# Kernel tuning notes

Hardware: AMD Instinct MI355X
Metric: run time of the kernel (lower is better)

The kernel has to match this reference:

```python
import jax, jax.numpy as jnp
import numpy as np

N_NODES = 10000
N_EDGES = 320000
D = 256
VOCAB = 28
NEG_SLOPE = 0.2


def _gat_conv(x, ei_src, ei_dst, W, a_src, a_dst, b):
    """PyG GATConv with heads=1, concat=True, self-loops already in ei."""
    h = x @ W                                  # [N, D]
    alpha_s = h @ a_src                        # [N]
    alpha_d = h @ a_dst                        # [N]
    logits = jax.nn.leaky_relu(alpha_s[ei_src] + alpha_d[ei_dst], NEG_SLOPE)  # [E]
    # numerically stable edge softmax per destination node
    m = jax.ops.segment_max(logits, ei_dst, num_segments=N_NODES)
    e = jnp.exp(logits - m[ei_dst])
    denom = jax.ops.segment_sum(e, ei_dst, num_segments=N_NODES)
    alpha = e / denom[ei_dst]                  # [E]
    msgs = alpha[:, None] * h[ei_src]          # [E, D]
    out = jax.ops.segment_sum(msgs, ei_dst, num_segments=N_NODES)
    return out + b


def setup_inputs() -> dict:
    key = jax.random.key(0)
    ks = jax.random.split(key, 16)
    x = jax.random.randint(ks[0], (N_NODES, 1), 0, VOCAB, dtype=jnp.int64)
    edge_index = jax.random.randint(ks[1], (2, N_EDGES), 0, N_NODES, dtype=jnp.int64)
    edge_attr = jax.random.uniform(ks[2], (N_EDGES,), dtype=jnp.float32)
    sc = 1.0 / np.sqrt(D)
    inp = {"x": x, "edge_index": edge_index, "edge_attr": edge_attr,
           "emb": jax.random.normal(ks[3], (VOCAB, D), jnp.float32)}
    for i, k0 in enumerate([4, 7, 10]):
        l = i + 1
        inp[f"W{l}"] = jax.random.normal(ks[k0], (D, D), jnp.float32) * sc
        inp[f"a_src{l}"] = jax.random.normal(ks[k0 + 1], (D,), jnp.float32) * sc
        inp[f"a_dst{l}"] = jax.random.normal(ks[k0 + 2], (D,), jnp.float32) * sc
        inp[f"b{l}"] = jnp.zeros((D,), jnp.float32)
    return inp


def reference(x, edge_index, edge_attr, emb,
              W1, a_src1, a_dst1, b1,
              W2, a_src2, a_dst2, b2,
              W3, a_src3, a_dst3, b3):
    # edge_attr is ignored by GATConv (edge_dim=None), matching PyG behavior.
    # add self loops (PyG default add_self_loops=True)
    loops = jnp.arange(N_NODES, dtype=edge_index.dtype)
    ei_src = jnp.concatenate([edge_index[0], loops])
    ei_dst = jnp.concatenate([edge_index[1], loops])

    h = emb[x.squeeze(-1)]                     # [N, D]
    h = jax.nn.relu(_gat_conv(h, ei_src, ei_dst, W1, a_src1, a_dst1, b1)) + h
    h = jax.nn.relu(_gat_conv(h, ei_src, ei_dst, W2, a_src2, a_dst2, b2)) + h
    out = jax.nn.relu(_gat_conv(h, ei_src, ei_dst, W3, a_src3, a_dst3, b3)) + h
    return out
```

## Files before the change

### kernel.cpp

```cpp
#include <hip/hip_runtime.h>
#include <hip/hip_bf16.h>

#define N_NODES 10000
#define N_EDGES 320000
#define E_TOT (N_EDGES + N_NODES)
#define D 256
#define VOCAB 28
#define NEG 0.2f
#define CAP 96

typedef __attribute__((ext_vector_type(8))) short bf16x8;
typedef __attribute__((ext_vector_type(4))) float f32x4;

__device__ inline float blo(unsigned u) { return __uint_as_float(u << 16); }
__device__ inline float bhi(unsigned u) { return __uint_as_float(u & 0xFFFF0000u); }
__device__ inline unsigned short f2bu(float x) {
  __hip_bfloat16 b = __float2bfloat16(x);
  return *reinterpret_cast<unsigned short*>(&b);
}

__global__ __launch_bounds__(256) void scatter_kernel(const int* __restrict__ ei,
                                                      int* __restrict__ counts,
                                                      int* __restrict__ csr) {
  int e = blockIdx.x * 256 + threadIdx.x;
  if (e >= E_TOT) return;
  int src, dst;
  if (e < N_EDGES) { src = ei[e]; dst = ei[N_EDGES + e]; }
  else             { src = e - N_EDGES; dst = src; }
  int pos = atomicAdd(&counts[dst], 1);
  csr[dst * CAP + pos] = src;
}

__global__ __launch_bounds__(256) void convw_kernel(const float* __restrict__ W0,
                                                    const float* __restrict__ W1,
                                                    const float* __restrict__ W2,
                                                    const float* __restrict__ emb,
                                                    unsigned short* __restrict__ T0,
                                                    unsigned short* __restrict__ T1,
                                                    unsigned short* __restrict__ T2,
                                                    unsigned short* __restrict__ emb_b,
                                                    float4* __restrict__ zbase) {
  __shared__ float t[64][65];
  int tid = threadIdx.x;
  if (blockIdx.x >= 49) {
    zbase[(blockIdx.x - 49) * 256 + tid] = float4{0.f, 0.f, 0.f, 0.f};
    return;
  }
  if (blockIdx.x == 48) {
    for (int i = tid; i < VOCAB * D; i += 256) emb_b[i] = f2bu(emb[i]);
    return;
  }
  int l = blockIdx.x >> 4;
  const float* W = (l == 0) ? W0 : (l == 1) ? W1 : W2;
  unsigned short* Wt = (l == 0) ? T0 : (l == 1) ? T1 : T2;
  int sub = blockIdx.x & 15;
  int bk = (sub & 3) * 64;
  int bn = (sub >> 2) * 64;
  int row = tid >> 2;
  int cq = (tid & 3) * 16;
#pragma unroll
  for (int i = 0; i < 4; ++i) {
    float4 v = *reinterpret_cast<const float4*>(W + (size_t)(bk + row) * D + bn + cq + i * 4);
    t[row][cq + i * 4 + 0] = v.x; t[row][cq + i * 4 + 1] = v.y;
    t[row][cq + i * 4 + 2] = v.z; t[row][cq + i * 4 + 3] = v.w;
  }
  __syncthreads();
#pragma unroll
  for (int i = 0; i < 16; ++i)
    Wt[(size_t)(bn + row) * D + bk + cq + i] = f2bu(t[cq + i][row]);
}

__global__ __launch_bounds__(256) void gemm_kernel(const unsigned short* __restrict__ Asrc,
                                                   const int* __restrict__ xv,
                                                   const unsigned short* __restrict__ emb_b,
                                                   const unsigned short* __restrict__ Bt,
                                                   unsigned short* __restrict__ C,
                                                   const float* __restrict__ a_src,
                                                   const float* __restrict__ a_dst,
                                                   float* __restrict__ al_s,
                                                   float* __restrict__ al_d) {
  __shared__ unsigned short As[64][264];
  __shared__ unsigned short Bs[64][264];
  __shared__ int xs[64];
  int t = threadIdx.x;
  int bm = blockIdx.x * 64;
  int bn = blockIdx.y * 64;
  int lane = t & 63, wid = t >> 6;
  int wr = (wid >> 1) * 32, wc = (wid & 1) * 32;
  int fr = lane & 15, fk = (lane >> 4) * 8;

  if (xv && t < 64) {
    int gr = bm + t;
    xs[t] = (gr < N_NODES) ? xv[gr] : 0;
  }
  if (xv) __syncthreads();

#pragma unroll
  for (int c = t; c < 2048; c += 256) {
    int row = c >> 5, cc = (c & 31) * 8;
    int gr = bm + row;
    uint4 v = {0u, 0u, 0u, 0u};
    if (gr < N_NODES) {
      const unsigned short* src = xv ? (emb_b + (size_t)xs[row] * D)
                                     : (Asrc + (size_t)gr * D);
      v = *reinterpret_cast<const uint4*>(src + cc);
    }
    *reinterpret_cast<uint4*>(&As[row][cc]) = v;
    uint4 w = *reinterpret_cast<const uint4*>(Bt + (size_t)(bn + row) * D + cc);
    *reinterpret_cast<uint4*>(&Bs[row][cc]) = w;
  }
  __syncthreads();

  f32x4 acc[2][2] = {};
#pragma unroll
  for (int ks = 0; ks < 8; ++ks) {
    bf16x8 a0 = *reinterpret_cast<const bf16x8*>(&As[wr + fr][ks * 32 + fk]);
    bf16x8 a1 = *reinterpret_cast<const bf16x8*>(&As[wr + 16 + fr][ks * 32 + fk]);
    bf16x8 b0 = *reinterpret_cast<const bf16x8*>(&Bs[wc + fr][ks * 32 + fk]);
    bf16x8 b1 = *reinterpret_cast<const bf16x8*>(&Bs[wc + 16 + fr][ks * 32 + fk]);
    acc[0][0] = __builtin_amdgcn_mfma_f32_16x16x32_bf16(a0, b0, acc[0][0], 0, 0, 0);
    acc[0][1] = __builtin_amdgcn_mfma_f32_16x16x32_bf16(a0, b1, acc[0][1], 0, 0, 0);
    acc[1][0] = __builtin_amdgcn_mfma_f32_16x16x32_bf16(a1, b0, acc[1][0], 0, 0, 0);
    acc[1][1] = __builtin_amdgcn_mfma_f32_16x16x32_bf16(a1, b1, acc[1][1], 0, 0, 0);
  }

  int orow = (lane >> 4) * 4;
#pragma unroll
  for (int m = 0; m < 2; ++m)
#pragma unroll
    for (int n = 0; n < 2; ++n)
#pragma unroll
      for (int r = 0; r < 4; ++r) {
        int gr = bm + wr + m * 16 + orow + r;
        if (gr < N_NODES)
          C[(size_t)gr * D + bn + wc + n * 16 + fr] = f2bu(acc[m][n][r]);
      }
  float as0 = a_src[bn + wc + fr];
  float as1 = a_src[bn + wc + 16 + fr];
  float ad0 = a_dst[bn + wc + fr];
  float ad1 = a_dst[bn + wc + 16 + fr];
#pragma unroll
  for (int m = 0; m < 2; ++m)
#pragma unroll
    for (int r = 0; r < 4; ++r) {
      float vs = acc[m][0][r] * as0 + acc[m][1][r] * as1;
      float vd = acc[m][0][r] * ad0 + acc[m][1][r] * ad1;
#pragma unroll
      for (int off = 8; off; off >>= 1) {
        vs += __shfl_xor(vs, off);
        vd += __shfl_xor(vd, off);
      }
      if ((lane & 15) == 0) {
        int gr = bm + wr + m * 16 + orow + r;
        if (gr < N_NODES) {
          atomicAdd(&al_s[gr], vs);
          atomicAdd(&al_d[gr], vd);
        }
      }
    }
}

__global__ __launch_bounds__(256) void agg_kernel(const int* __restrict__ csr,
                                                  const int* __restrict__ counts,
                                                  const float* __restrict__ al_s,
                                                  const float* __restrict__ al_d,
                                                  const unsigned short* __restrict__ hlin,
                                                  const float* __restrict__ bias,
                                                  const float* __restrict__ h_prev,
                                                  const int* __restrict__ xv,
                                                  const float* __restrict__ emb,
                                                  float* __restrict__ out_f,
                                                  unsigned short* __restrict__ out_b) {
  __shared__ int   ssh[4][CAP];
  __shared__ float wsh[4][CAP];
  int wid = threadIdx.x >> 6, lane = threadIdx.x & 63;
  int dst = blockIdx.x * 4 + wid;
  if (dst >= N_NODES) return;
  int cnt = counts[dst];
  const int* rowp = csr + (size_t)dst * CAP;
  float ad = al_d[dst];

  float m = -1e30f;
  for (int j = lane; j < cnt; j += 64) {
    int s = rowp[j];
    ssh[wid][j] = s;
    float v = al_s[s] + ad;
    v = (v >= 0.f) ? v : NEG * v;
    wsh[wid][j] = v;
    m = fmaxf(m, v);
  }
#pragma unroll
  for (int off = 32; off; off >>= 1) m = fmaxf(m, __shfl_xor(m, off));

  float denom = 0.f;
  for (int j = lane; j < cnt; j += 64) {
    float w = __expf(wsh[wid][j] - m);
    wsh[wid][j] = w;
    denom += w;
  }
#pragma unroll
  for (int off = 32; off; off >>= 1) denom += __shfl_xor(denom, off);
  float inv = 1.0f / denom;

  int half = lane >> 5, fl = lane & 31;
  const unsigned short* hb_base = hlin + fl * 8;
  float a0 = 0.f, a1 = 0.f, a2 = 0.f, a3 = 0.f;
  float a4 = 0.f, a5 = 0.f, a6 = 0.f, a7 = 0.f;
  int j = 0;
  for (; j + 8 <= cnt; j += 8) {
    int s0 = ssh[wid][j + 0 + half];
    int s1 = ssh[wid][j + 2 + half];
    int s2 = ssh[wid][j + 4 + half];
    int s3 = ssh[wid][j + 6 + half];
    float w0 = wsh[wid][j + 0 + half];
    float w1 = wsh[wid][j + 2 + half];
    float w2 = wsh[wid][j + 4 + half];
    float w3 = wsh[wid][j + 6 + half];
    uint4 q0 = *reinterpret_cast<const uint4*>(hb_base + (size_t)s0 * D);
    uint4 q1 = *reinterpret_cast<const uint4*>(hb_base + (size_t)s1 * D);
    uint4 q2 = *reinterpret_cast<const uint4*>(hb_base + (size_t)s2 * D);
    uint4 q3 = *reinterpret_cast<const uint4*>(hb_base + (size_t)s3 * D);
    a0 += w0 * blo(q0.x); a1 += w0 * bhi(q0.x); a2 += w0 * blo(q0.y); a3 += w0 * bhi(q0.y);
    a4 += w0 * blo(q0.z); a5 += w0 * bhi(q0.z); a6 += w0 * blo(q0.w); a7 += w0 * bhi(q0.w);
    a0 += w1 * blo(q1.x); a1 += w1 * bhi(q1.x); a2 += w1 * blo(q1.y); a3 += w1 * bhi(q1.y);
    a4 += w1 * blo(q1.z); a5 += w1 * bhi(q1.z); a6 += w1 * blo(q1.w); a7 += w1 * bhi(q1.w);
    a0 += w2 * blo(q2.x); a1 += w2 * bhi(q2.x); a2 += w2 * blo(q2.y); a3 += w2 * bhi(q2.y);
    a4 += w2 * blo(q2.z); a5 += w2 * bhi(q2.z); a6 += w2 * blo(q2.w); a7 += w2 * bhi(q2.w);
    a0 += w3 * blo(q3.x); a1 += w3 * bhi(q3.x); a2 += w3 * blo(q3.y); a3 += w3 * bhi(q3.y);
    a4 += w3 * blo(q3.z); a5 += w3 * bhi(q3.z); a6 += w3 * blo(q3.w); a7 += w3 * bhi(q3.w);
  }
  for (; j < cnt; j += 2) {
    int jj = j + half;
    bool valid = jj < cnt;
    int s0 = ssh[wid][valid ? jj : 0];
    float w0 = valid ? wsh[wid][jj] : 0.f;
    uint4 q0 = *reinterpret_cast<const uint4*>(hb_base + (size_t)s0 * D);
    a0 += w0 * blo(q0.x); a1 += w0 * bhi(q0.x); a2 += w0 * blo(q0.y); a3 += w0 * bhi(q0.y);
    a4 += w0 * blo(q0.z); a5 += w0 * bhi(q0.z); a6 += w0 * blo(q0.w); a7 += w0 * bhi(q0.w);
  }
  a0 += __shfl_xor(a0, 32); a1 += __shfl_xor(a1, 32);
  a2 += __shfl_xor(a2, 32); a3 += __shfl_xor(a3, 32);
  a4 += __shfl_xor(a4, 32); a5 += __shfl_xor(a5, 32);
  a6 += __shfl_xor(a6, 32); a7 += __shfl_xor(a7, 32);
  float b0 = half ? a4 : a0, b1 = half ? a5 : a1;
  float b2 = half ? a6 : a2, b3 = half ? a7 : a3;
  int fb = fl * 8 + half * 4;
  const float* hp_row = h_prev ? (h_prev + (size_t)dst * D)
                               : (emb + (size_t)xv[dst] * D);
  float4 bb = *reinterpret_cast<const float4*>(bias + fb);
  float4 hp = *reinterpret_cast<const float4*>(hp_row + fb);
  float o0 = fmaxf(b0 * inv + bb.x, 0.f) + hp.x;
  float o1 = fmaxf(b1 * inv + bb.y, 0.f) + hp.y;
  float o2 = fmaxf(b2 * inv + bb.z, 0.f) + hp.z;
  float o3 = fmaxf(b3 * inv + bb.w, 0.f) + hp.w;
  float4 o = {o0, o1, o2, o3};
  *reinterpret_cast<float4*>(out_f + (size_t)dst * D + fb) = o;
  if (out_b) {
    uint2 p;
    p.x = (unsigned)f2bu(o0) | ((unsigned)f2bu(o1) << 16);
    p.y = (unsigned)f2bu(o2) | ((unsigned)f2bu(o3) << 16);
    *reinterpret_cast<uint2*>(out_b + (size_t)dst * D + fb) = p;
  }
}

extern "C" void kernel_launch(void* const* d_in, const int* in_sizes, int n_in,
                              void* d_out, int out_size, void* d_ws, size_t ws_size,
                              hipStream_t stream) {
  const int*   x   = (const int*)d_in[0];
  const int*   ei  = (const int*)d_in[1];
  const float* emb = (const float*)d_in[3];
  const float* W[3]    = {(const float*)d_in[4],  (const float*)d_in[8],  (const float*)d_in[12]};
  const float* asrc[3] = {(const float*)d_in[5],  (const float*)d_in[9],  (const float*)d_in[13]};
  const float* adst[3] = {(const float*)d_in[6],  (const float*)d_in[10], (const float*)d_in[14]};
  const float* bias[3] = {(const float*)d_in[7],  (const float*)d_in[11], (const float*)d_in[15]};

  char* ws = (char*)d_ws;
  float*          h    = (float*)(ws);
  unsigned short* hb   = (unsigned short*)(ws + 10240000);
  unsigned short* hlin = (unsigned short*)(ws + 15360000);
  unsigned short* Wt[3] = {(unsigned short*)(ws + 20480000),
                           (unsigned short*)(ws + 20611072),
                           (unsigned short*)(ws + 20742144)};
  float* al_s[3] = {(float*)(ws + 20873216), (float*)(ws + 20914176), (float*)(ws + 20955136)};
  float* al_d[3] = {(float*)(ws + 20996096), (float*)(ws + 21037056), (float*)(ws + 21078016)};
  int* counts = (int*)(ws + 21118976);
  int* csr    = (int*)(ws + 21241856);
  unsigned short* emb_b = (unsigned short*)(ws + 25081856);

  convw_kernel<<<119, 256, 0, stream>>>(W[0], W[1], W[2], emb,
                                        Wt[0], Wt[1], Wt[2], emb_b,
                                        (float4*)(ws + 20873216));

  scatter_kernel<<<(E_TOT + 255) / 256, 256, 0, stream>>>(ei, counts, csr);

  dim3 gemm_grid((N_NODES + 63) / 64, D / 64);
  for (int l = 0; l < 3; ++l) {
    const unsigned short* Ain = (l == 0) ? (const unsigned short*)nullptr : hb;
    const int* xg = (l == 0) ? x : (const int*)nullptr;
    gemm_kernel<<<gemm_grid, 256, 0, stream>>>(Ain, xg, emb_b, Wt[l], hlin,
                                               asrc[l], adst[l], al_s[l], al_d[l]);
    float* outp = (l == 2) ? (float*)d_out : h;
    unsigned short* outb = (l == 2) ? (unsigned short*)nullptr : hb;
    const float* hp = (l == 0) ? (const float*)nullptr : h;
    agg_kernel<<<(N_NODES + 3) / 4, 256, 0, stream>>>(csr, counts, al_s[l], al_d[l],
                                                      hlin, bias[l], hp, x, emb,
                                                      outp, outb);
  }
}
```

Measured before the change: 137.6 us.

## Fuse all stages into one cooperative persistent kernel with grid syncs

Replaces the eight separate launches (weight conversion, CSR scatter, three GEMM plus aggregation pairs) with a single cooperative persistent kernel that separates phases with grid.sync. The first GEMM runs alongside the edge scatter on disjoint block subsets. The GEMM tile now loops over K in 64-wide chunks with a smaller shared buffer, which lowers LDS use and raises occupancy but adds syncthreads per K step. The aim is to remove launch gaps and tail effects, in exchange for the cost of grid-wide barriers and a fixed grid size.

```diff
diff --git a/kernel.cpp b/kernel.cpp
--- a/kernel.cpp
+++ b/kernel.cpp
@@ -1,5 +1,8 @@
 #include <hip/hip_runtime.h>
 #include <hip/hip_bf16.h>
+#include <hip/hip_cooperative_groups.h>
+
+namespace cg = cooperative_groups;
 
 #define N_NODES 10000
 #define N_EDGES 320000
@@ -8,6 +11,10 @@
 #define VOCAB 28
 #define NEG 0.2f
 #define CAP 96
+#define NTILE_M 157
+#define NTILES (NTILE_M * 4)
+#define NGROUP 2500
+#define SMEM_BYTES 18688
 
 typedef __attribute__((ext_vector_type(8))) short bf16x8;
 typedef __attribute__((ext_vector_type(4))) float f32x4;
@@ -19,109 +26,73 @@
   return *reinterpret_cast<unsigned short*>(&b);
 }
 
-__global__ __launch_bounds__(256) void scatter_kernel(const int* __restrict__ ei,
-                                                      int* __restrict__ counts,
-                                                      int* __restrict__ csr) {
-  int e = blockIdx.x * 256 + threadIdx.x;
-  if (e >= E_TOT) return;
-  int src, dst;
-  if (e < N_EDGES) { src = ei[e]; dst = ei[N_EDGES + e]; }
-  else             { src = e - N_EDGES; dst = src; }
-  int pos = atomicAdd(&counts[dst], 1);
-  csr[dst * CAP + pos] = src;
-}
-
-__global__ __launch_bounds__(256) void convw_kernel(const float* __restrict__ W0,
-                                                    const float* __restrict__ W1,
-                                                    const float* __restrict__ W2,
-                                                    const float* __restrict__ emb,
-                                                    unsigned short* __restrict__ T0,
-                                                    unsigned short* __restrict__ T1,
-                                                    unsigned short* __restrict__ T2,
-                                                    unsigned short* __restrict__ emb_b,
-                                                    float4* __restrict__ zbase) {
-  __shared__ float t[64][65];
-  int tid = threadIdx.x;
-  if (blockIdx.x >= 49) {
-    zbase[(blockIdx.x - 49) * 256 + tid] = float4{0.f, 0.f, 0.f, 0.f};
-    return;
-  }
-  if (blockIdx.x == 48) {
-    for (int i = tid; i < VOCAB * D; i += 256) emb_b[i] = f2bu(emb[i]);
-    return;
-  }
-  int l = blockIdx.x >> 4;
-  const float* W = (l == 0) ? W0 : (l == 1) ? W1 : W2;
-  unsigned short* Wt = (l == 0) ? T0 : (l == 1) ? T1 : T2;
-  int sub = blockIdx.x & 15;
-  int bk = (sub & 3) * 64;
-  int bn = (sub >> 2) * 64;
-  int row = tid >> 2;
-  int cq = (tid & 3) * 16;
-#pragma unroll
-  for (int i = 0; i < 4; ++i) {
-    float4 v = *reinterpret_cast<const float4*>(W + (size_t)(bk + row) * D + bn + cq + i * 4);
-    t[row][cq + i * 4 + 0] = v.x; t[row][cq + i * 4 + 1] = v.y;
-    t[row][cq + i * 4 + 2] = v.z; t[row][cq + i * 4 + 3] = v.w;
-  }
-  __syncthreads();
-#pragma unroll
-  for (int i = 0; i < 16; ++i)
-    Wt[(size_t)(bn + row) * D + bk + cq + i] = f2bu(t[cq + i][row]);
-}
-
-__global__ __launch_bounds__(256) void gemm_kernel(const unsigned short* __restrict__ Asrc,
-                                                   const int* __restrict__ xv,
-                                                   const unsigned short* __restrict__ emb_b,
-                                                   const unsigned short* __restrict__ Bt,
-                                                   unsigned short* __restrict__ C,
-                                                   const float* __restrict__ a_src,
-                                                   const float* __restrict__ a_dst,
-                                                   float* __restrict__ al_s,
-                                                   float* __restrict__ al_d) {
-  __shared__ unsigned short As[64][264];
-  __shared__ unsigned short Bs[64][264];
-  __shared__ int xs[64];
+struct MegaArgs {
+  const int* x; const int* ei;
+  const float *emb, *W0, *W1, *W2;
+  const float *as0, *ad0, *b0, *as1, *ad1, *b1, *as2, *ad2, *b2;
+  unsigned short *T0, *T1, *T2, *emb_b, *hb, *hlin;
+  float *h;
+  float *als0, *ald0, *als1, *ald1, *als2, *ald2;
+  int *counts, *csr;
+  float4* zbase;
+  float* dout;
+};
+
+__device__ void gemm_tile(int tile, const unsigned short* __restrict__ Asrc,
+                          const int* __restrict__ xv,
+                          const unsigned short* __restrict__ emb_b,
+                          const unsigned short* __restrict__ Bt,
+                          unsigned short* __restrict__ C,
+                          const float* __restrict__ a_src, const float* __restrict__ a_dst,
+                          float* __restrict__ al_s, float* __restrict__ al_d,
+                          char* smem) {
+  unsigned short (*As)[72] = (unsigned short(*)[72])smem;
+  unsigned short (*Bs)[72] = (unsigned short(*)[72])(smem + 9216);
+  int* xs = (int*)(smem + 18432);
   int t = threadIdx.x;
-  int bm = blockIdx.x * 64;
-  int bn = blockIdx.y * 64;
+  int bm = (tile % NTILE_M) * 64;
+  int bn = (tile / NTILE_M) * 64;
   int lane = t & 63, wid = t >> 6;
   int wr = (wid >> 1) * 32, wc = (wid & 1) * 32;
   int fr = lane & 15, fk = (lane >> 4) * 8;
 
-  if (xv && t < 64) {
-    int gr = bm + t;
-    xs[t] = (gr < N_NODES) ? xv[gr] : 0;
-  }
-  if (xv) __syncthreads();
-
-#pragma unroll
-  for (int c = t; c < 2048; c += 256) {
-    int row = c >> 5, cc = (c & 31) * 8;
-    int gr = bm + row;
-    uint4 v = {0u, 0u, 0u, 0u};
-    if (gr < N_NODES) {
-      const unsigned short* src = xv ? (emb_b + (size_t)xs[row] * D)
-                                     : (Asrc + (size_t)gr * D);
-      v = *reinterpret_cast<const uint4*>(src + cc);
-    }
-    *reinterpret_cast<uint4*>(&As[row][cc]) = v;
-    uint4 w = *reinterpret_cast<const uint4*>(Bt + (size_t)(bn + row) * D + cc);
-    *reinterpret_cast<uint4*>(&Bs[row][cc]) = w;
-  }
-  __syncthreads();
+  if (xv) {
+    if (t < 64) {
+      int gr = bm + t;
+      xs[t] = (gr < N_NODES) ? xv[gr] : 0;
+    }
+    __syncthreads();
+  }
 
   f32x4 acc[2][2] = {};
-#pragma unroll
-  for (int ks = 0; ks < 8; ++ks) {
-    bf16x8 a0 = *reinterpret_cast<const bf16x8*>(&As[wr + fr][ks * 32 + fk]);
-    bf16x8 a1 = *reinterpret_cast<const bf16x8*>(&As[wr + 16 + fr][ks * 32 + fk]);
-    bf16x8 b0 = *reinterpret_cast<const bf16x8*>(&Bs[wc + fr][ks * 32 + fk]);
-    bf16x8 b1 = *reinterpret_cast<const bf16x8*>(&Bs[wc + 16 + fr][ks * 32 + fk]);
-    acc[0][0] = __builtin_amdgcn_mfma_f32_16x16x32_bf16(a0, b0, acc[0][0], 0, 0, 0);
-    acc[0][1] = __builtin_amdgcn_mfma_f32_16x16x32_bf16(a0, b1, acc[0][1], 0, 0, 0);
-    acc[1][0] = __builtin_amdgcn_mfma_f32_16x16x32_bf16(a1, b0, acc[1][0], 0, 0, 0);
-    acc[1][1] = __builtin_amdgcn_mfma_f32_16x16x32_bf16(a1, b1, acc[1][1], 0, 0, 0);
+  for (int k0 = 0; k0 < D; k0 += 64) {
+#pragma unroll
+    for (int c = t; c < 512; c += 256) {
+      int row = c >> 3, cc = (c & 7) * 8;
+      int gr = bm + row;
+      uint4 v = {0u, 0u, 0u, 0u};
+      if (gr < N_NODES) {
+        const unsigned short* src = xv ? (emb_b + (size_t)xs[row] * D)
+                                       : (Asrc + (size_t)gr * D);
+        v = *reinterpret_cast<const uint4*>(src + k0 + cc);
+      }
+      *reinterpret_cast<uint4*>(&As[row][cc]) = v;
+      uint4 w = *reinterpret_cast<const uint4*>(Bt + (size_t)(bn + row) * D + k0 + cc);
+      *reinterpret_cast<uint4*>(&Bs[row][cc]) = w;
+    }
+    __syncthreads();
+#pragma unroll
+    for (int ks = 0; ks < 2; ++ks) {
+      bf16x8 a0 = *reinterpret_cast<const bf16x8*>(&As[wr + fr][ks * 32 + fk]);
+      bf16x8 a1 = *reinterpret_cast<const bf16x8*>(&As[wr + 16 + fr][ks * 32 + fk]);
+      bf16x8 b0 = *reinterpret_cast<const bf16x8*>(&Bs[wc + fr][ks * 32 + fk]);
+      bf16x8 b1 = *reinterpret_cast<const bf16x8*>(&Bs[wc + 16 + fr][ks * 32 + fk]);
+      acc[0][0] = __builtin_amdgcn_mfma_f32_16x16x32_bf16(a0, b0, acc[0][0], 0, 0, 0);
+      acc[0][1] = __builtin_amdgcn_mfma_f32_16x16x32_bf16(a0, b1, acc[0][1], 0, 0, 0);
+      acc[1][0] = __builtin_amdgcn_mfma_f32_16x16x32_bf16(a1, b0, acc[1][0], 0, 0, 0);
+      acc[1][1] = __builtin_amdgcn_mfma_f32_16x16x32_bf16(a1, b1, acc[1][1], 0, 0, 0);
+    }
+    __syncthreads();
   }
 
   int orow = (lane >> 4) * 4;
@@ -160,22 +131,17 @@
     }
 }
 
-__global__ __launch_bounds__(256) void agg_kernel(const int* __restrict__ csr,
-                                                  const int* __restrict__ counts,
-                                                  const float* __restrict__ al_s,
-                                                  const float* __restrict__ al_d,
-                                                  const unsigned short* __restrict__ hlin,
-                                                  const float* __restrict__ bias,
-                                                  const float* __restrict__ h_prev,
-                                                  const int* __restrict__ xv,
-                                                  const float* __restrict__ emb,
-                                                  float* __restrict__ out_f,
-                                                  unsigned short* __restrict__ out_b) {
-  __shared__ int   ssh[4][CAP];
-  __shared__ float wsh[4][CAP];
+__device__ void agg_group(int g, const int* __restrict__ csr, const int* __restrict__ counts,
+                          const float* __restrict__ al_s, const float* __restrict__ al_d,
+                          const unsigned short* __restrict__ hlin,
+                          const float* __restrict__ bias, const float* __restrict__ h_prev,
+                          const int* __restrict__ xv, const float* __restrict__ emb,
+                          float* __restrict__ out_f, unsigned short* __restrict__ out_b,
+                          char* smem) {
+  int (*ssh)[CAP] = (int(*)[CAP])smem;
+  float (*wsh)[CAP] = (float(*)[CAP])(smem + 4 * CAP * 4);
   int wid = threadIdx.x >> 6, lane = threadIdx.x & 63;
-  int dst = blockIdx.x * 4 + wid;
-  if (dst >= N_NODES) return;
+  int dst = g * 4 + wid;
   int cnt = counts[dst];
   const int* rowp = csr + (size_t)dst * CAP;
   float ad = al_d[dst];
@@ -263,47 +229,126 @@
   }
 }
 
+__global__ __launch_bounds__(256) void mega_kernel(MegaArgs a) {
+  __shared__ __align__(16) char smem[SMEM_BYTES];
+  cg::grid_group grid = cg::this_grid();
+  const int bid = blockIdx.x;
+  const int G = gridDim.x;
+  const int tid = threadIdx.x;
+
+  if (bid < 48) {
+    float (*t)[65] = (float(*)[65])smem;
+    int l = bid >> 4;
+    const float* W = (l == 0) ? a.W0 : (l == 1) ? a.W1 : a.W2;
+    unsigned short* Wt = (l == 0) ? a.T0 : (l == 1) ? a.T1 : a.T2;
+    int sub = bid & 15;
+    int bk = (sub & 3) * 64;
+    int bn = (sub >> 2) * 64;
+    int row = tid >> 2;
+    int cq = (tid & 3) * 16;
+#pragma unroll
+    for (int i = 0; i < 4; ++i) {
+      float4 v = *reinterpret_cast<const float4*>(W + (size_t)(bk + row) * D + bn + cq + i * 4);
+      t[row][cq + i * 4 + 0] = v.x; t[row][cq + i * 4 + 1] = v.y;
+      t[row][cq + i * 4 + 2] = v.z; t[row][cq + i * 4 + 3] = v.w;
+    }
+    __syncthreads();
+#pragma unroll
+    for (int i = 0; i < 16; ++i)
+      Wt[(size_t)(bn + row) * D + bk + cq + i] = f2bu(t[cq + i][row]);
+  } else if (bid == 48) {
+    for (int i = tid; i < VOCAB * D; i += 256) a.emb_b[i] = f2bu(a.emb[i]);
+  } else {
+    for (int i = (bid - 49) * 256 + tid; i < 17920; i += (G - 49) * 256)
+      a.zbase[i] = float4{0.f, 0.f, 0.f, 0.f};
+  }
+  grid.sync();
+
+  {
+    int Gg = (3 * G) / 4;
+    if (Gg > NTILES) Gg = NTILES;
+    if (bid < Gg) {
+      for (int tile = bid; tile < NTILES; tile += Gg)
+        gemm_tile(tile, nullptr, a.x, a.emb_b, a.T0, a.hlin,
+                  a.as0, a.ad0, a.als0, a.ald0, smem);
+    } else {
+      int nb = G - Gg;
+      for (int e = (bid - Gg) * 256 + tid; e < E_TOT; e += nb * 256) {
+        int src, dst;
+        if (e < N_EDGES) { src = a.ei[e]; dst = a.ei[N_EDGES + e]; }
+        else             { src = e - N_EDGES; dst = src; }
+        int pos = atomicAdd(&a.counts[dst], 1);
+        a.csr[dst * CAP + pos] = src;
+      }
+    }
+  }
+  grid.sync();
+
+  for (int g = bid; g < NGROUP; g += G)
+    agg_group(g, a.csr, a.counts, a.als0, a.ald0, a.hlin, a.b0,
+              nullptr, a.x, a.emb, a.h, a.hb, smem);
+  grid.sync();
+
+  for (int tile = bid; tile < NTILES; tile += G)
+    gemm_tile(tile, a.hb, nullptr, a.emb_b, a.T1, a.hlin,
+              a.as1, a.ad1, a.als1, a.ald1, smem);
+  grid.sync();
+
+  for (int g = bid; g < NGROUP; g += G)
+    agg_group(g, a.csr, a.counts, a.als1, a.ald1, a.hlin, a.b1,
+              a.h, a.x, a.emb, a.h, a.hb, smem);
+  grid.sync();
+
+  for (int tile = bid; tile < NTILES; tile += G)
+    gemm_tile(tile, a.hb, nullptr, a.emb_b, a.T2, a.hlin,
+              a.as2, a.ad2, a.als2, a.ald2, smem);
+  grid.sync();
+
+  for (int g = bid; g < NGROUP; g += G)
+    agg_group(g, a.csr, a.counts, a.als2, a.ald2, a.hlin, a.b2,
+              a.h, a.x, a.emb, a.dout, nullptr, smem);
+}
+
 extern "C" void kernel_launch(void* const* d_in, const int* in_sizes, int n_in,
                               void* d_out, int out_size, void* d_ws, size_t ws_size,
                               hipStream_t stream) {
-  const int*   x   = (const int*)d_in[0];
-  const int*   ei  = (const int*)d_in[1];
-  const float* emb = (const float*)d_in[3];
-  const float* W[3]    = {(const float*)d_in[4],  (const float*)d_in[8],  (const float*)d_in[12]};
-  const float* asrc[3] = {(const float*)d_in[5],  (const float*)d_in[9],  (const float*)d_in[13]};
-  const float* adst[3] = {(const float*)d_in[6],  (const float*)d_in[10], (const float*)d_in[14]};
-  const float* bias[3] = {(const float*)d_in[7],  (const float*)d_in[11], (const float*)d_in[15]};
-
   char* ws = (char*)d_ws;
-  float*          h    = (float*)(ws);
-  unsigned short* hb   = (unsigned short*)(ws + 10240000);
-  unsigned short* hlin = (unsigned short*)(ws + 15360000);
-  unsigned short* Wt[3] = {(unsigned short*)(ws + 20480000),
-                           (unsigned short*)(ws + 20611072),
-                           (unsigned short*)(ws + 20742144)};
-  float* al_s[3] = {(float*)(ws + 20873216), (float*)(ws + 20914176), (float*)(ws + 20955136)};
-  float* al_d[3] = {(float*)(ws + 20996096), (float*)(ws + 21037056), (float*)(ws + 21078016)};
-  int* counts = (int*)(ws + 21118976);
-  int* csr    = (int*)(ws + 21241856);
-  unsigned short* emb_b = (unsigned short*)(ws + 25081856);
-
-  convw_kernel<<<119, 256, 0, stream>>>(W[0], W[1], W[2], emb,
-                                        Wt[0], Wt[1], Wt[2], emb_b,
-                                        (float4*)(ws + 20873216));
-
-  scatter_kernel<<<(E_TOT + 255) / 256, 256, 0, stream>>>(ei, counts, csr);
-
-  dim3 gemm_grid((N_NODES + 63) / 64, D / 64);
-  for (int l = 0; l < 3; ++l) {
-    const unsigned short* Ain = (l == 0) ? (const unsigned short*)nullptr : hb;
-    const int* xg = (l == 0) ? x : (const int*)nullptr;
-    gemm_kernel<<<gemm_grid, 256, 0, stream>>>(Ain, xg, emb_b, Wt[l], hlin,
-                                               asrc[l], adst[l], al_s[l], al_d[l]);
-    float* outp = (l == 2) ? (float*)d_out : h;
-    unsigned short* outb = (l == 2) ? (unsigned short*)nullptr : hb;
-    const float* hp = (l == 0) ? (const float*)nullptr : h;
-    agg_kernel<<<(N_NODES + 3) / 4, 256, 0, stream>>>(csr, counts, al_s[l], al_d[l],
-                                                      hlin, bias[l], hp, x, emb,
-                                                      outp, outb);
-  }
-}
+  MegaArgs a;
+  a.x   = (const int*)d_in[0];
+  a.ei  = (const int*)d_in[1];
+  a.emb = (const float*)d_in[3];
+  a.W0 = (const float*)d_in[4];  a.as0 = (const float*)d_in[5];
+  a.ad0 = (const float*)d_in[6]; a.b0 = (const float*)d_in[7];
+  a.W1 = (const float*)d_in[8];  a.as1 = (const float*)d_in[9];
+  a.ad1 = (const float*)d_in[10]; a.b1 = (const float*)d_in[11];
+  a.W2 = (const float*)d_in[12]; a.as2 = (const float*)d_in[13];
+  a.ad2 = (const float*)d_in[14]; a.b2 = (const float*)d_in[15];
+
+  a.h     = (float*)(ws);
+  a.hb    = (unsigned short*)(ws + 10240000);
+  a.hlin  = (unsigned short*)(ws + 15360000);
+  a.T0    = (unsigned short*)(ws + 20480000);
+  a.T1    = (unsigned short*)(ws + 20611072);
+  a.T2    = (unsigned short*)(ws + 20742144);
+  a.als0  = (float*)(ws + 20873216);
+  a.als1  = (float*)(ws + 20914176);
+  a.als2  = (float*)(ws + 20955136);
+  a.ald0  = (float*)(ws + 20996096);
+  a.ald1  = (float*)(ws + 21037056);
+  a.ald2  = (float*)(ws + 21078016);
+  a.counts = (int*)(ws + 21118976);
+  a.zbase  = (float4*)(ws + 20873216);
+  a.csr    = (int*)(ws + 21241856);
+  a.emb_b  = (unsigned short*)(ws + 25081856);
+  a.dout   = (float*)d_out;
+
+  int bpc = 0;
+  hipError_t err = hipOccupancyMaxActiveBlocksPerMultiprocessor(&bpc, mega_kernel, 256, 0);
+  if (err != hipSuccess || bpc < 1) bpc = 2;
+  int G = bpc * 256;
+  if (G > 2048) G = 2048;
+  if (G < 256) G = 256;
+
+  void* kargs[] = { &a };
+  hipLaunchCooperativeKernel(mega_kernel, dim3(G), dim3(256), kargs, 0, stream);
+}
```

Measured after the change: 491.4 us. 257% more time.

## Loop GEMM over all output column tiles per block, drop attention-score atomics

Applied to the files above, without the earlier changes.

Each GEMM block now loads its 64-row A tile once and loops over the four 64-column B tiles, instead of launching a 2D grid that reloads A for each column tile. The per-row attention dot products are accumulated in registers, reduced through shared memory, and written directly, which removes the atomicAdds and the need to zero al_s/al_d. As a result the convw kernel launches fewer blocks and only zeroes counts. The trade-off is a grid 4x smaller (157 blocks), which may underfill the GPU, plus serialized B loads with extra barriers inside each block.

```diff
diff --git a/kernel.cpp b/kernel.cpp
--- a/kernel.cpp
+++ b/kernel.cpp
@@ -8,6 +8,7 @@
 #define VOCAB 28
 #define NEG 0.2f
 #define CAP 96
+#define NBLK 157
 
 typedef __attribute__((ext_vector_type(8))) short bf16x8;
 typedef __attribute__((ext_vector_type(4))) float f32x4;
@@ -81,19 +82,23 @@
                                                    float* __restrict__ al_d) {
   __shared__ unsigned short As[64][264];
   __shared__ unsigned short Bs[64][264];
+  __shared__ float red_s[8][32];
+  __shared__ float red_d[8][32];
   __shared__ int xs[64];
   int t = threadIdx.x;
   int bm = blockIdx.x * 64;
-  int bn = blockIdx.y * 64;
   int lane = t & 63, wid = t >> 6;
-  int wr = (wid >> 1) * 32, wc = (wid & 1) * 32;
+  int wrb = (wid >> 1) * 32, wcb = (wid & 1) * 32;
   int fr = lane & 15, fk = (lane >> 4) * 8;
-
-  if (xv && t < 64) {
-    int gr = bm + t;
-    xs[t] = (gr < N_NODES) ? xv[gr] : 0;
-  }
-  if (xv) __syncthreads();
+  int orow = (lane >> 4) * 4;
+
+  if (xv) {
+    if (t < 64) {
+      int gr = bm + t;
+      xs[t] = (gr < N_NODES) ? xv[gr] : 0;
+    }
+    __syncthreads();
+  }
 
 #pragma unroll
   for (int c = t; c < 2048; c += 256) {
@@ -106,58 +111,79 @@
       v = *reinterpret_cast<const uint4*>(src + cc);
     }
     *reinterpret_cast<uint4*>(&As[row][cc]) = v;
-    uint4 w = *reinterpret_cast<const uint4*>(Bt + (size_t)(bn + row) * D + cc);
-    *reinterpret_cast<uint4*>(&Bs[row][cc]) = w;
-  }
-  __syncthreads();
-
-  f32x4 acc[2][2] = {};
-#pragma unroll
-  for (int ks = 0; ks < 8; ++ks) {
-    bf16x8 a0 = *reinterpret_cast<const bf16x8*>(&As[wr + fr][ks * 32 + fk]);
-    bf16x8 a1 = *reinterpret_cast<const bf16x8*>(&As[wr + 16 + fr][ks * 32 + fk]);
-    bf16x8 b0 = *reinterpret_cast<const bf16x8*>(&Bs[wc + fr][ks * 32 + fk]);
-    bf16x8 b1 = *reinterpret_cast<const bf16x8*>(&Bs[wc + 16 + fr][ks * 32 + fk]);
-    acc[0][0] = __builtin_amdgcn_mfma_f32_16x16x32_bf16(a0, b0, acc[0][0], 0, 0, 0);
-    acc[0][1] = __builtin_amdgcn_mfma_f32_16x16x32_bf16(a0, b1, acc[0][1], 0, 0, 0);
-    acc[1][0] = __builtin_amdgcn_mfma_f32_16x16x32_bf16(a1, b0, acc[1][0], 0, 0, 0);
-    acc[1][1] = __builtin_amdgcn_mfma_f32_16x16x32_bf16(a1, b1, acc[1][1], 0, 0, 0);
-  }
-
-  int orow = (lane >> 4) * 4;
+  }
+
+  float aS[2][4] = {}, aD[2][4] = {};
+  for (int bn = 0; bn < 4; ++bn) {
+#pragma unroll
+    for (int c = t; c < 2048; c += 256) {
+      int row = c >> 5, cc = (c & 31) * 8;
+      uint4 w = *reinterpret_cast<const uint4*>(Bt + (size_t)(bn * 64 + row) * D + cc);
+      *reinterpret_cast<uint4*>(&Bs[row][cc]) = w;
+    }
+    __syncthreads();
+
+    f32x4 acc[2][2] = {};
+#pragma unroll
+    for (int ks = 0; ks < 8; ++ks) {
+      bf16x8 a0 = *reinterpret_cast<const bf16x8*>(&As[wrb + fr][ks * 32 + fk]);
+      bf16x8 a1 = *reinterpret_cast<const bf16x8*>(&As[wrb + 16 + fr][ks * 32 + fk]);
+      bf16x8 b0 = *reinterpret_cast<const bf16x8*>(&Bs[wcb + fr][ks * 32 + fk]);
+      bf16x8 b1 = *reinterpret_cast<const bf16x8*>(&Bs[wcb + 16 + fr][ks * 32 + fk]);
+      acc[0][0] = __builtin_amdgcn_mfma_f32_16x16x32_bf16(a0, b0, acc[0][0], 0, 0, 0);
+      acc[0][1] = __builtin_amdgcn_mfma_f32_16x16x32_bf16(a0, b1, acc[0][1], 0, 0, 0);
+      acc[1][0] = __builtin_amdgcn_mfma_f32_16x16x32_bf16(a1, b0, acc[1][0], 0, 0, 0);
+      acc[1][1] = __builtin_amdgcn_mfma_f32_16x16x32_bf16(a1, b1, acc[1][1], 0, 0, 0);
+    }
+
+#pragma unroll
+    for (int m = 0; m < 2; ++m)
+#pragma unroll
+      for (int n = 0; n < 2; ++n)
+#pragma unroll
+        for (int r = 0; r < 4; ++r) {
+          int gr = bm + wrb + m * 16 + orow + r;
+          if (gr < N_NODES)
+            C[(size_t)gr * D + bn * 64 + wcb + n * 16 + fr] = f2bu(acc[m][n][r]);
+        }
+    float as0 = a_src[bn * 64 + wcb + fr];
+    float as1 = a_src[bn * 64 + wcb + 16 + fr];
+    float ad0 = a_dst[bn * 64 + wcb + fr];
+    float ad1 = a_dst[bn * 64 + wcb + 16 + fr];
+#pragma unroll
+    for (int m = 0; m < 2; ++m)
+#pragma unroll
+      for (int r = 0; r < 4; ++r) {
+        aS[m][r] += acc[m][0][r] * as0 + acc[m][1][r] * as1;
+        aD[m][r] += acc[m][0][r] * ad0 + acc[m][1][r] * ad1;
+      }
+    __syncthreads();
+  }
+
 #pragma unroll
   for (int m = 0; m < 2; ++m)
 #pragma unroll
-    for (int n = 0; n < 2; ++n)
-#pragma unroll
-      for (int r = 0; r < 4; ++r) {
-        int gr = bm + wr + m * 16 + orow + r;
-        if (gr < N_NODES)
-          C[(size_t)gr * D + bn + wc + n * 16 + fr] = f2bu(acc[m][n][r]);
-      }
-  float as0 = a_src[bn + wc + fr];
-  float as1 = a_src[bn + wc + 16 + fr];
-  float ad0 = a_dst[bn + wc + fr];
-  float ad1 = a_dst[bn + wc + 16 + fr];
-#pragma unroll
-  for (int m = 0; m < 2; ++m)
-#pragma unroll
     for (int r = 0; r < 4; ++r) {
-      float vs = acc[m][0][r] * as0 + acc[m][1][r] * as1;
-      float vd = acc[m][0][r] * ad0 + acc[m][1][r] * ad1;
+      float vs = aS[m][r], vd = aD[m][r];
 #pragma unroll
       for (int off = 8; off; off >>= 1) {
         vs += __shfl_xor(vs, off);
         vd += __shfl_xor(vd, off);
       }
-      if ((lane & 15) == 0) {
-        int gr = bm + wr + m * 16 + orow + r;
-        if (gr < N_NODES) {
-          atomicAdd(&al_s[gr], vs);
-          atomicAdd(&al_d[gr], vd);
-        }
+      if (fr == 0) {
+        red_s[wid][m * 16 + orow + r] = vs;
+        red_d[wid][m * 16 + orow + r] = vd;
       }
     }
+  __syncthreads();
+  if (t < 64) {
+    int gr = bm + t;
+    if (gr < N_NODES) {
+      int p = (t >> 5) * 2, lr = t & 31;
+      al_s[gr] = red_s[p][lr] + red_s[p + 1][lr];
+      al_d[gr] = red_d[p][lr] + red_d[p + 1][lr];
+    }
+  }
 }
 
 __global__ __launch_bounds__(256) void agg_kernel(const int* __restrict__ csr,
@@ -287,18 +313,17 @@
   int* csr    = (int*)(ws + 21241856);
   unsigned short* emb_b = (unsigned short*)(ws + 25081856);
 
-  convw_kernel<<<119, 256, 0, stream>>>(W[0], W[1], W[2], emb,
-                                        Wt[0], Wt[1], Wt[2], emb_b,
-                                        (float4*)(ws + 20873216));
+  convw_kernel<<<59, 256, 0, stream>>>(W[0], W[1], W[2], emb,
+                                       Wt[0], Wt[1], Wt[2], emb_b,
+                                       (float4*)counts);
 
   scatter_kernel<<<(E_TOT + 255) / 256, 256, 0, stream>>>(ei, counts, csr);
 
-  dim3 gemm_grid((N_NODES + 63) / 64, D / 64);
   for (int l = 0; l < 3; ++l) {
     const unsigned short* Ain = (l == 0) ? (const unsigned short*)nullptr : hb;
     const int* xg = (l == 0) ? x : (const int*)nullptr;
-    gemm_kernel<<<gemm_grid, 256, 0, stream>>>(Ain, xg, emb_b, Wt[l], hlin,
-                                               asrc[l], adst[l], al_s[l], al_d[l]);
+    gemm_kernel<<<NBLK, 256, 0, stream>>>(Ain, xg, emb_b, Wt[l], hlin,
+                                          asrc[l], adst[l], al_s[l], al_d[l]);
     float* outp = (l == 2) ? (float*)d_out : h;
     unsigned short* outb = (l == 2) ? (unsigned short*)nullptr : hb;
     const float* hp = (l == 0) ? (const float*)nullptr : h;
```

New measurement: 140.2 us. About the same (+1.9%).

## Precompute W·a vectors and compute attention scores in aggregation epilogue

Applied to the files above, without the earlier changes.

Attention logits are now computed as h·(W a) instead of (hW)·a. The products W·a_src and W·a_dst are precomputed in a merged prep kernel; layer 1 scores come from a vocab lookup, and layers 2 and 3 scores come from the previous aggregation's fp32 output via a wave reduction. This removes the atomicAdd epilogue and the zeroing it needed from the GEMM. The GEMM also switches from a full-K shared tile to K-chunks of 64 with smaller LDS, which should raise occupancy but adds syncs. Scores now use fp32 h rather than the bf16 GEMM output, which slightly changes the numerics.

```diff
diff --git a/kernel.cpp b/kernel.cpp
--- a/kernel.cpp
+++ b/kernel.cpp
@@ -17,6 +17,105 @@
 __device__ inline unsigned short f2bu(float x) {
   __hip_bfloat16 b = __float2bfloat16(x);
   return *reinterpret_cast<unsigned short*>(&b);
+}
+
+__global__ __launch_bounds__(256) void prep_kernel(const float* __restrict__ W0,
+                                                   const float* __restrict__ W1,
+                                                   const float* __restrict__ W2,
+                                                   const float* __restrict__ emb,
+                                                   const float* __restrict__ as1,
+                                                   const float* __restrict__ ad1,
+                                                   const float* __restrict__ as2,
+                                                   const float* __restrict__ ad2,
+                                                   const float* __restrict__ as3,
+                                                   const float* __restrict__ ad3,
+                                                   const int* __restrict__ x,
+                                                   unsigned short* __restrict__ T0,
+                                                   unsigned short* __restrict__ T1,
+                                                   unsigned short* __restrict__ T2,
+                                                   unsigned short* __restrict__ emb_b,
+                                                   float4* __restrict__ zbase,
+                                                   float* __restrict__ waS2,
+                                                   float* __restrict__ waD2,
+                                                   float* __restrict__ waS3,
+                                                   float* __restrict__ waD3,
+                                                   float* __restrict__ al1_s,
+                                                   float* __restrict__ al1_d) {
+  int tid = threadIdx.x;
+  int bid = blockIdx.x;
+  if (bid < 48) {
+    __shared__ float t[64][65];
+    int l = bid >> 4;
+    const float* W = (l == 0) ? W0 : (l == 1) ? W1 : W2;
+    unsigned short* Wt = (l == 0) ? T0 : (l == 1) ? T1 : T2;
+    int sub = bid & 15;
+    int bk = (sub & 3) * 64;
+    int bn = (sub >> 2) * 64;
+    int row = tid >> 2;
+    int cq = (tid & 3) * 16;
+#pragma unroll
+    for (int i = 0; i < 4; ++i) {
+      float4 v = *reinterpret_cast<const float4*>(W + (size_t)(bk + row) * D + bn + cq + i * 4);
+      t[row][cq + i * 4 + 0] = v.x; t[row][cq + i * 4 + 1] = v.y;
+      t[row][cq + i * 4 + 2] = v.z; t[row][cq + i * 4 + 3] = v.w;
+    }
+    __syncthreads();
+#pragma unroll
+    for (int i = 0; i < 16; ++i)
+      Wt[(size_t)(bn + row) * D + bk + cq + i] = f2bu(t[cq + i][row]);
+  } else if (bid == 48) {
+    for (int i = tid; i < VOCAB * D; i += 256) emb_b[i] = f2bu(emb[i]);
+  } else if (bid < 59) {
+    zbase[(bid - 49) * 256 + tid] = float4{0.f, 0.f, 0.f, 0.f};
+  } else if (bid == 59 || bid == 60) {
+    const float* W = (bid == 59) ? W1 : W2;
+    const float* as = (bid == 59) ? as2 : as3;
+    const float* ad = (bid == 59) ? ad2 : ad3;
+    float* oS = (bid == 59) ? waS2 : waS3;
+    float* oD = (bid == 59) ? waD2 : waD3;
+    float s = 0.f, d = 0.f;
+    const float* row = W + (size_t)tid * D;
+    for (int n = 0; n < D; ++n) {
+      float w = row[n];
+      s += w * as[n];
+      d += w * ad[n];
+    }
+    oS[tid] = s; oD[tid] = d;
+  } else {
+    __shared__ float ws1[256], wd1[256], avs[VOCAB], avd[VOCAB];
+    {
+      float s = 0.f, d = 0.f;
+      const float* row = W0 + (size_t)tid * D;
+      for (int n = 0; n < D; ++n) {
+        float w = row[n];
+        s += w * as1[n];
+        d += w * ad1[n];
+      }
+      ws1[tid] = s; wd1[tid] = d;
+    }
+    __syncthreads();
+    int wid = tid >> 6, lane = tid & 63;
+    for (int t = wid; t < VOCAB; t += 4) {
+      float ps = 0.f, pd = 0.f;
+      for (int k = lane; k < D; k += 64) {
+        float e = emb[(size_t)t * D + k];
+        ps += e * ws1[k];
+        pd += e * wd1[k];
+      }
+#pragma unroll
+      for (int off = 32; off; off >>= 1) {
+        ps += __shfl_xor(ps, off);
+        pd += __shfl_xor(pd, off);
+      }
+      if (lane == 0) { avs[t] = ps; avd[t] = pd; }
+    }
+    __syncthreads();
+    for (int n = tid; n < N_NODES; n += 256) {
+      int t = x[n];
+      al1_s[n] = avs[t];
+      al1_d[n] = avd[t];
+    }
+  }
 }
 
 __global__ __launch_bounds__(256) void scatter_kernel(const int* __restrict__ ei,
@@ -31,56 +130,13 @@
   csr[dst * CAP + pos] = src;
 }
 
-__global__ __launch_bounds__(256) void convw_kernel(const float* __restrict__ W0,
-                                                    const float* __restrict__ W1,
-                                                    const float* __restrict__ W2,
-                                                    const float* __restrict__ emb,
-                                                    unsigned short* __restrict__ T0,
-                                                    unsigned short* __restrict__ T1,
-                                                    unsigned short* __restrict__ T2,
-                                                    unsigned short* __restrict__ emb_b,
-                                                    float4* __restrict__ zbase) {
-  __shared__ float t[64][65];
-  int tid = threadIdx.x;
-  if (blockIdx.x >= 49) {
-    zbase[(blockIdx.x - 49) * 256 + tid] = float4{0.f, 0.f, 0.f, 0.f};
-    return;
-  }
-  if (blockIdx.x == 48) {
-    for (int i = tid; i < VOCAB * D; i += 256) emb_b[i] = f2bu(emb[i]);
-    return;
-  }
-  int l = blockIdx.x >> 4;
-  const float* W = (l == 0) ? W0 : (l == 1) ? W1 : W2;
-  unsigned short* Wt = (l == 0) ? T0 : (l == 1) ? T1 : T2;
-  int sub = blockIdx.x & 15;
-  int bk = (sub & 3) * 64;
-  int bn = (sub >> 2) * 64;
-  int row = tid >> 2;
-  int cq = (tid & 3) * 16;
-#pragma unroll
-  for (int i = 0; i < 4; ++i) {
-    float4 v = *reinterpret_cast<const float4*>(W + (size_t)(bk + row) * D + bn + cq + i * 4);
-    t[row][cq + i * 4 + 0] = v.x; t[row][cq + i * 4 + 1] = v.y;
-    t[row][cq + i * 4 + 2] = v.z; t[row][cq + i * 4 + 3] = v.w;
-  }
-  __syncthreads();
-#pragma unroll
-  for (int i = 0; i < 16; ++i)
-    Wt[(size_t)(bn + row) * D + bk + cq + i] = f2bu(t[cq + i][row]);
-}
-
 __global__ __launch_bounds__(256) void gemm_kernel(const unsigned short* __restrict__ Asrc,
                                                    const int* __restrict__ xv,
                                                    const unsigned short* __restrict__ emb_b,
                                                    const unsigned short* __restrict__ Bt,
-                                                   unsigned short* __restrict__ C,
-                                                   const float* __restrict__ a_src,
-                                                   const float* __restrict__ a_dst,
-                                                   float* __restrict__ al_s,
-                                                   float* __restrict__ al_d) {
-  __shared__ unsigned short As[64][264];
-  __shared__ unsigned short Bs[64][264];
+                                                   unsigned short* __restrict__ C) {
+  __shared__ unsigned short As[64][72];
+  __shared__ unsigned short Bs[64][72];
   __shared__ int xs[64];
   int t = threadIdx.x;
   int bm = blockIdx.x * 64;
@@ -89,39 +145,43 @@
   int wr = (wid >> 1) * 32, wc = (wid & 1) * 32;
   int fr = lane & 15, fk = (lane >> 4) * 8;
 
-  if (xv && t < 64) {
-    int gr = bm + t;
-    xs[t] = (gr < N_NODES) ? xv[gr] : 0;
-  }
-  if (xv) __syncthreads();
-
-#pragma unroll
-  for (int c = t; c < 2048; c += 256) {
-    int row = c >> 5, cc = (c & 31) * 8;
-    int gr = bm + row;
-    uint4 v = {0u, 0u, 0u, 0u};
-    if (gr < N_NODES) {
-      const unsigned short* src = xv ? (emb_b + (size_t)xs[row] * D)
-                                     : (Asrc + (size_t)gr * D);
-      v = *reinterpret_cast<const uint4*>(src + cc);
-    }
-    *reinterpret_cast<uint4*>(&As[row][cc]) = v;
-    uint4 w = *reinterpret_cast<const uint4*>(Bt + (size_t)(bn + row) * D + cc);
-    *reinterpret_cast<uint4*>(&Bs[row][cc]) = w;
-  }
-  __syncthreads();
+  if (xv) {
+    if (t < 64) {
+      int gr = bm + t;
+      xs[t] = (gr < N_NODES) ? xv[gr] : 0;
+    }
+    __syncthreads();
+  }
 
   f32x4 acc[2][2] = {};
-#pragma unroll
-  for (int ks = 0; ks < 8; ++ks) {
-    bf16x8 a0 = *reinterpret_cast<const bf16x8*>(&As[wr + fr][ks * 32 + fk]);
-    bf16x8 a1 = *reinterpret_cast<const bf16x8*>(&As[wr + 16 + fr][ks * 32 + fk]);
-    bf16x8 b0 = *reinterpret_cast<const bf16x8*>(&Bs[wc + fr][ks * 32 + fk]);
-    bf16x8 b1 = *reinterpret_cast<const bf16x8*>(&Bs[wc + 16 + fr][ks * 32 + fk]);
-    acc[0][0] = __builtin_amdgcn_mfma_f32_16x16x32_bf16(a0, b0, acc[0][0], 0, 0, 0);
-    acc[0][1] = __builtin_amdgcn_mfma_f32_16x16x32_bf16(a0, b1, acc[0][1], 0, 0, 0);
-    acc[1][0] = __builtin_amdgcn_mfma_f32_16x16x32_bf16(a1, b0, acc[1][0], 0, 0, 0);
-    acc[1][1] = __builtin_amdgcn_mfma_f32_16x16x32_bf16(a1, b1, acc[1][1], 0, 0, 0);
+  for (int k0 = 0; k0 < D; k0 += 64) {
+#pragma unroll
+    for (int c = t; c < 512; c += 256) {
+      int row = c >> 3, cc = (c & 7) * 8;
+      int gr = bm + row;
+      uint4 v = {0u, 0u, 0u, 0u};
+      if (gr < N_NODES) {
+        const unsigned short* src = xv ? (emb_b + (size_t)xs[row] * D)
+                                       : (Asrc + (size_t)gr * D);
+        v = *reinterpret_cast<const uint4*>(src + k0 + cc);
+      }
+      *reinterpret_cast<uint4*>(&As[row][cc]) = v;
+      uint4 w = *reinterpret_cast<const uint4*>(Bt + (size_t)(bn + row) * D + k0 + cc);
+      *reinterpret_cast<uint4*>(&Bs[row][cc]) = w;
+    }
+    __syncthreads();
+#pragma unroll
+    for (int ks = 0; ks < 2; ++ks) {
+      bf16x8 a0 = *reinterpret_cast<const bf16x8*>(&As[wr + fr][ks * 32 + fk]);
+      bf16x8 a1 = *reinterpret_cast<const bf16x8*>(&As[wr + 16 + fr][ks * 32 + fk]);
+      bf16x8 b0 = *reinterpret_cast<const bf16x8*>(&Bs[wc + fr][ks * 32 + fk]);
+      bf16x8 b1 = *reinterpret_cast<const bf16x8*>(&Bs[wc + 16 + fr][ks * 32 + fk]);
+      acc[0][0] = __builtin_amdgcn_mfma_f32_16x16x32_bf16(a0, b0, acc[0][0], 0, 0, 0);
+      acc[0][1] = __builtin_amdgcn_mfma_f32_16x16x32_bf16(a0, b1, acc[0][1], 0, 0, 0);
+      acc[1][0] = __builtin_amdgcn_mfma_f32_16x16x32_bf16(a1, b0, acc[1][0], 0, 0, 0);
+      acc[1][1] = __builtin_amdgcn_mfma_f32_16x16x32_bf16(a1, b1, acc[1][1], 0, 0, 0);
+    }
+    __syncthreads();
   }
 
   int orow = (lane >> 4) * 4;
@@ -135,29 +195,6 @@
         if (gr < N_NODES)
           C[(size_t)gr * D + bn + wc + n * 16 + fr] = f2bu(acc[m][n][r]);
       }
-  float as0 = a_src[bn + wc + fr];
-  float as1 = a_src[bn + wc + 16 + fr];
-  float ad0 = a_dst[bn + wc + fr];
-  float ad1 = a_dst[bn + wc + 16 + fr];
-#pragma unroll
-  for (int m = 0; m < 2; ++m)
-#pragma unroll
-    for (int r = 0; r < 4; ++r) {
-      float vs = acc[m][0][r] * as0 + acc[m][1][r] * as1;
-      float vd = acc[m][0][r] * ad0 + acc[m][1][r] * ad1;
-#pragma unroll
-      for (int off = 8; off; off >>= 1) {
-        vs += __shfl_xor(vs, off);
-        vd += __shfl_xor(vd, off);
-      }
-      if ((lane & 15) == 0) {
-        int gr = bm + wr + m * 16 + orow + r;
-        if (gr < N_NODES) {
-          atomicAdd(&al_s[gr], vs);
-          atomicAdd(&al_d[gr], vd);
-        }
-      }
-    }
 }
 
 __global__ __launch_bounds__(256) void agg_kernel(const int* __restrict__ csr,
@@ -170,7 +207,11 @@
                                                   const int* __restrict__ xv,
                                                   const float* __restrict__ emb,
                                                   float* __restrict__ out_f,
-                                                  unsigned short* __restrict__ out_b) {
+                                                  unsigned short* __restrict__ out_b,
+                                                  const float* __restrict__ waS_n,
+                                                  const float* __restrict__ waD_n,
+                                                  float* __restrict__ aln_s,
+                                                  float* __restrict__ aln_d) {
   __shared__ int   ssh[4][CAP];
   __shared__ float wsh[4][CAP];
   int wid = threadIdx.x >> 6, lane = threadIdx.x & 63;
@@ -261,6 +302,18 @@
     p.y = (unsigned)f2bu(o2) | ((unsigned)f2bu(o3) << 16);
     *reinterpret_cast<uint2*>(out_b + (size_t)dst * D + fb) = p;
   }
+  if (waS_n) {
+    float4 s4 = *reinterpret_cast<const float4*>(waS_n + fb);
+    float4 d4 = *reinterpret_cast<const float4*>(waD_n + fb);
+    float ps = o0 * s4.x + o1 * s4.y + o2 * s4.z + o3 * s4.w;
+    float pd = o0 * d4.x + o1 * d4.y + o2 * d4.z + o3 * d4.w;
+#pragma unroll
+    for (int off = 32; off; off >>= 1) {
+      ps += __shfl_xor(ps, off);
+      pd += __shfl_xor(pd, off);
+    }
+    if (lane == 0) { aln_s[dst] = ps; aln_d[dst] = pd; }
+  }
 }
 
 extern "C" void kernel_launch(void* const* d_in, const int* in_sizes, int n_in,
@@ -286,24 +339,33 @@
   int* counts = (int*)(ws + 21118976);
   int* csr    = (int*)(ws + 21241856);
   unsigned short* emb_b = (unsigned short*)(ws + 25081856);
-
-  convw_kernel<<<119, 256, 0, stream>>>(W[0], W[1], W[2], emb,
-                                        Wt[0], Wt[1], Wt[2], emb_b,
-                                        (float4*)(ws + 20873216));
+  float* waS2 = (float*)(ws + 25096192);
+  float* waD2 = (float*)(ws + 25097216);
+  float* waS3 = (float*)(ws + 25098240);
+  float* waD3 = (float*)(ws + 25099264);
+
+  prep_kernel<<<62, 256, 0, stream>>>(W[0], W[1], W[2], emb,
+                                      asrc[0], adst[0], asrc[1], adst[1], asrc[2], adst[2],
+                                      x, Wt[0], Wt[1], Wt[2], emb_b,
+                                      (float4*)counts, waS2, waD2, waS3, waD3,
+                                      al_s[0], al_d[0]);
 
   scatter_kernel<<<(E_TOT + 255) / 256, 256, 0, stream>>>(ei, counts, csr);
 
-  dim3 gemm_grid((N_NODES + 63) / 64, D / 64);
+  dim3 gemm_grid(157, 4);
   for (int l = 0; l < 3; ++l) {
     const unsigned short* Ain = (l == 0) ? (const unsigned short*)nullptr : hb;
     const int* xg = (l == 0) ? x : (const int*)nullptr;
-    gemm_kernel<<<gemm_grid, 256, 0, stream>>>(Ain, xg, emb_b, Wt[l], hlin,
-                                               asrc[l], adst[l], al_s[l], al_d[l]);
+    gemm_kernel<<<gemm_grid, 256, 0, stream>>>(Ain, xg, emb_b, Wt[l], hlin);
     float* outp = (l == 2) ? (float*)d_out : h;
     unsigned short* outb = (l == 2) ? (unsigned short*)nullptr : hb;
     const float* hp = (l == 0) ? (const float*)nullptr : h;
+    const float* wsn = (l == 0) ? waS2 : (l == 1) ? waS3 : (const float*)nullptr;
+    const float* wdn = (l == 0) ? waD2 : (l == 1) ? waD3 : (const float*)nullptr;
+    float* alns = (l < 2) ? al_s[l + 1] : (float*)nullptr;
+    float* alnd = (l < 2) ? al_d[l + 1] : (float*)nullptr;
     agg_kernel<<<(N_NODES + 3) / 4, 256, 0, stream>>>(csr, counts, al_s[l], al_d[l],
                                                       hlin, bias[l], hp, x, emb,
-                                                      outp, outb);
-  }
-}
+                                                      outp, outb, wsn, wdn, alns, alnd);
+  }
+}
```

New measurement: 135.1 us. No clear change (-1.8%).
